# Performance work log

Hardware: AMD Instinct MI355X
Metric: run time of the kernel (lower is better)

Reference implementation:

```python
import jax, jax.numpy as jnp
import numpy as np

N_NODES = 20000   # graph nodes (rows of x)
N_EDGES = 40000
NUM_ENT = 300000  # node_count: embedding table rows
EMB_DIM = 64
D = 2 * EMB_DIM           # self.emb_dim = 128
SE = int(0.36 * D)        # s_emb_dim = 46
TE = D - SE               # t_emb_dim = 82
F = 256                   # raw feature cols of x
HID = 128                 # n_hidden
OUT = 2


def setup_inputs() -> dict:
    key = jax.random.key(0)
    ks = jax.random.split(key, 24)
    def nrm(k, shape, fan_in):
        return jax.random.normal(k, shape, jnp.float32) / np.sqrt(fan_in)
    inp = {
        'x': jax.random.normal(ks[0], (N_NODES, F), jnp.float32),
        'heads': jax.random.randint(ks[1], (N_EDGES,), 0, NUM_ENT),
        'rels': jax.random.randint(ks[2], (N_EDGES,), 0, 4),
        'tails': jax.random.randint(ks[3], (N_EDGES,), 0, NUM_ENT),
        'weeks': jax.random.uniform(ks[4], (N_EDGES,), jnp.float32),
        'edge_src': jnp.sort(jax.random.randint(ks[5], (N_EDGES,), 0, N_NODES)),
        'edge_dst': jax.random.randint(ks[6], (N_EDGES,), 0, N_NODES),
        'node_type': jax.random.randint(ks[7], (N_NODES,), 0, 5),
        'edge_type': jax.random.randint(ks[8], (N_EDGES,), 0, 4),
        'edge_index': jax.random.randint(ks[9], (2, N_EDGES), 0, N_NODES),
        # learned parameters
        'ent_embs': nrm(ks[10], (NUM_ENT, SE), SE),
        'rel_embs': nrm(ks[11], (4, D), D),
        'w_freq': nrm(ks[12], (NUM_ENT, TE), TE),
        'w_phi': nrm(ks[13], (NUM_ENT, TE), TE),
        'w_amp': nrm(ks[14], (NUM_ENT, TE), TE),
        'Wih': nrm(ks[15], (4 * D, D), D),
        'Whh': nrm(ks[16], (4 * D, D), D),
        'bih': jnp.zeros((4 * D,), jnp.float32),
        'bhh': jnp.zeros((4 * D,), jnp.float32),
        'fc1_w': nrm(ks[17], (HID, F + D), F + D),
        'fc1_b': jnp.zeros((HID,), jnp.float32),
        'ln_g': jnp.ones((HID,), jnp.float32),
        'ln_b': jnp.zeros((HID,), jnp.float32),
        'out_w': nrm(ks[18], (OUT, HID), HID),
        'out_b': jnp.zeros((OUT,), jnp.float32),
    }
    return inp


def _lstm_last_per_segment(pre, seg, Whh, bhh):
    """Run one LSTM over edges sorted by seg, resetting state at group
    boundaries; return per-step hidden states and the scatter index that
    selects the last step of each group (others map to dummy row N_NODES).
    pre: [E, 4D] precomputed x @ Wih^T + bih (sorted by seg)."""
    reset = jnp.concatenate([jnp.ones((1,), bool), seg[1:] != seg[:-1]])
    def step(carry, inp):
        h, c = carry
        p, r = inp
        h = jnp.where(r, 0.0, h)
        c = jnp.where(r, 0.0, c)
        gates = p + h @ Whh.T + bhh
        i, f, g, o = jnp.split(gates, 4, axis=-1)
        c = jax.nn.sigmoid(f) * c + jax.nn.sigmoid(i) * jnp.tanh(g)
        h = jax.nn.sigmoid(o) * jnp.tanh(c)
        return (h, c), h
    zero = jnp.zeros((D,), pre.dtype)
    _, hs = jax.lax.scan(step, (zero, zero), (pre, reset))
    is_last = jnp.concatenate([seg[1:] != seg[:-1], jnp.ones((1,), bool)])
    idx = jnp.where(is_last, seg, N_NODES)  # dummy row for non-last steps
    return hs, idx


def reference(x, heads, rels, tails, weeks, edge_src, edge_dst, node_type,
              edge_type, edge_index, ent_embs, rel_embs, w_freq, w_phi, w_amp,
              Wih, Whh, bih, bhh, fc1_w, fc1_b, ln_g, ln_b, out_w, out_b):
    week = weeks.reshape(-1, 1)  # [E,1]
    # getEmbeddings: static entity emb + diachronic (amp*sin(freq*t+phi)) part
    h_t = w_amp[heads] * jnp.sin(w_freq[heads] * week + w_phi[heads])
    t_t = w_amp[tails] * jnp.sin(w_freq[tails] * week + w_phi[tails])
    h = jnp.concatenate([ent_embs[heads], h_t], axis=1)  # [E, D]
    t = jnp.concatenate([ent_embs[tails], t_t], axis=1)  # [E, D]
    r = rel_embs[rels]                                    # [E, D]
    scores = h * r * t                                    # [E, D]

    # Ragged per-group LSTM (src groups, then dst groups overwrite), fused
    # as a single segment-reset scan per pass. Input projection hoisted.
    pre = scores @ Wih.T + bih  # [E, 4D]
    emb = jnp.zeros((N_NODES + 1, D), scores.dtype)
    perm_s = jnp.argsort(edge_src)  # stable
    hs, idx = _lstm_last_per_segment(pre[perm_s], edge_src[perm_s], Whh, bhh)
    emb = emb.at[idx].set(hs)
    perm_d = jnp.argsort(edge_dst)
    hs, idx = _lstm_last_per_segment(pre[perm_d], edge_dst[perm_d], Whh, bhh)
    emb = emb.at[idx].set(hs)
    emb = emb[:N_NODES]

    # (hgtconv2 omitted: GeneralConv source unavailable; treated as identity)
    xc = jnp.concatenate([x, emb], axis=1)  # mask = arange(N): all rows
    h1 = xc @ fc1_w.T + fc1_b
    mu = jnp.mean(h1, axis=-1, keepdims=True)
    var = jnp.mean((h1 - mu) ** 2, axis=-1, keepdims=True)
    h1 = (h1 - mu) / jnp.sqrt(var + 1e-5) * ln_g + ln_b
    h1 = jax.nn.relu(h1)  # dropout: eval mode, identity
    return h1 @ out_w.T + out_b
```

## Files before the change

kernel.cpp:

```cpp
#include <hip/hip_runtime.h>
#include <math.h>

#define N_NODES 20000
#define N_EDGES 40000
#define SE 46
#define TE 82
#define NBLK 79

typedef short  s16x8 __attribute__((ext_vector_type(8)));
typedef short  s16x4 __attribute__((ext_vector_type(4)));
typedef float  f32x4 __attribute__((ext_vector_type(4)));

__device__ __forceinline__ float sigf(float x){ return 1.0f/(1.0f+__expf(-x)); }
__device__ __forceinline__ float tanh_f(float x){ return 1.0f - 2.0f/(__expf(2.0f*x)+1.0f); }
__device__ __forceinline__ int perm_out(int i){ return (i&3)*128 + (i>>2); }
__device__ __forceinline__ unsigned short f2bf(float f){
  unsigned u = __builtin_bit_cast(unsigned, f);
  unsigned r = (u + 0x7fff + ((u>>16)&1)) >> 16;
  return (unsigned short)r;
}
__device__ __forceinline__ float bf2f(short s){
  unsigned u = ((unsigned)(unsigned short)s) << 16;
  return __builtin_bit_cast(float, u);
}

__global__ void k_prep(const float* __restrict__ Wih, const float* __restrict__ Whh,
                       const float* __restrict__ fc1w,
                       short* __restrict__ WihB, short* __restrict__ WhhB2,
                       short* __restrict__ fc1wbf){
  int idx = blockIdx.x*blockDim.x + threadIdx.x;
  if (idx < 65536){
    int i = idx >> 7, k = idx & 127;
    WihB[idx] = (short)f2bf(Wih[perm_out(i)*128 + k]);
  } else if (idx < 131072){
    int j = idx - 65536;
    WhhB2[j] = (short)f2bf(Whh[j]);
  } else if (idx < 180224){
    int j = idx - 131072;
    fc1wbf[j] = (short)f2bf(fc1w[j]);
  }
}

__global__ __launch_bounds__(256) void k_gather(
    const int* __restrict__ heads, const int* __restrict__ rels,
    const int* __restrict__ tails, const float* __restrict__ weeks,
    const float* __restrict__ ent, const float* __restrict__ rel_embs,
    const float* __restrict__ wfreq, const float* __restrict__ wphi,
    const float* __restrict__ wamp, short* __restrict__ scores){
  int c = blockIdx.x*256 + threadIdx.x;
  int e = c >> 4, d0 = (c & 15) << 3;
  int hd = heads[e], tl = tails[e], rl = rels[e];
  float wk = weeks[e];
  float hv[8], tv[8];
  if (d0 + 8 <= SE){
    const float* hp = ent + (size_t)hd*SE + d0;
    const float* tp = ent + (size_t)tl*SE + d0;
    #pragma unroll
    for (int j=0;j<4;j++){
      float2 a = *(const float2*)(hp + j*2); hv[2*j]=a.x; hv[2*j+1]=a.y;
      float2 b = *(const float2*)(tp + j*2); tv[2*j]=b.x; tv[2*j+1]=b.y;
    }
  } else if (d0 >= 48){
    int dt = d0 - SE;
    const float *hf = wfreq + (size_t)hd*TE + dt, *hp2 = wphi + (size_t)hd*TE + dt, *ha = wamp + (size_t)hd*TE + dt;
    const float *tf = wfreq + (size_t)tl*TE + dt, *tp2 = wphi + (size_t)tl*TE + dt, *ta = wamp + (size_t)tl*TE + dt;
    #pragma unroll
    for (int j=0;j<4;j++){
      float2 f_h = *(const float2*)(hf + j*2);
      float2 p_h = *(const float2*)(hp2 + j*2);
      float2 a_h = *(const float2*)(ha + j*2);
      float2 f_t = *(const float2*)(tf + j*2);
      float2 p_t = *(const float2*)(tp2 + j*2);
      float2 a_t = *(const float2*)(ta + j*2);
      hv[2*j]   = a_h.x*__sinf(f_h.x*wk + p_h.x);
      hv[2*j+1] = a_h.y*__sinf(f_h.y*wk + p_h.y);
      tv[2*j]   = a_t.x*__sinf(f_t.x*wk + p_t.x);
      tv[2*j+1] = a_t.y*__sinf(f_t.y*wk + p_t.y);
    }
  } else {
    #pragma unroll
    for (int j=0;j<8;j++){
      int d = 40 + j;
      if (d < SE){
        hv[j] = ent[(size_t)hd*SE + d];
        tv[j] = ent[(size_t)tl*SE + d];
      } else {
        int dt = d - SE;
        hv[j] = wamp[(size_t)hd*TE+dt]*__sinf(wfreq[(size_t)hd*TE+dt]*wk + wphi[(size_t)hd*TE+dt]);
        tv[j] = wamp[(size_t)tl*TE+dt]*__sinf(wfreq[(size_t)tl*TE+dt]*wk + wphi[(size_t)tl*TE+dt]);
      }
    }
  }
  const float* rp = rel_embs + rl*128 + d0;
  float4 r0 = *(const float4*)rp, r1 = *(const float4*)(rp+4);
  float rv[8] = {r0.x,r0.y,r0.z,r0.w, r1.x,r1.y,r1.z,r1.w};
  s16x8 o;
  #pragma unroll
  for (int j=0;j<8;j++) o[j] = (short)f2bf(hv[j]*rv[j]*tv[j]);
  *(s16x8*)(scores + (size_t)e*128 + d0) = o;
}

__global__ __launch_bounds__(256) void k_pregemm(
    const short* __restrict__ scores, const short* __restrict__ WihB,
    const float* __restrict__ bih, const float* __restrict__ bhh,
    short* __restrict__ pre2b){
  __shared__ char As[32*256];
  int e0 = blockIdx.x * 32;
  int tid = threadIdx.x;
  #pragma unroll
  for (int q=0;q<2;q++){
    int c = tid + 256*q;
    int el = c >> 4, k8 = c & 15;
    s16x8 v = *(const s16x8*)(scores + (size_t)(e0+el)*128 + k8*8);
    *(s16x8*)(As + ((el*256 + k8*16) ^ ((el&7)<<4))) = v;
  }
  __syncthreads();
  int lane = tid & 63, w = tid >> 6;
  int cl = lane & 15, kq = lane >> 4;
  s16x8 a[2][4];
  #pragma unroll
  for (int ks=0;ks<4;ks++){
    int kb = ks*64 + kq*16;
    a[0][ks] = *(const s16x8*)(As + (((cl   )*256 + kb) ^ ((cl&7)<<4)));
    a[1][ks] = *(const s16x8*)(As + (((cl+16)*256 + kb) ^ (((cl+16)&7)<<4)));
  }
  f32x4 D[2][8];
  #pragma unroll
  for (int m=0;m<2;m++)
    #pragma unroll
    for (int i=0;i<8;i++) D[m][i] = (f32x4){0.f,0.f,0.f,0.f};
  #pragma unroll
  for (int i=0;i<8;i++){
    int n = w*128 + i*16 + cl;
    const short* bp = WihB + (size_t)n*128 + kq*8;
    #pragma unroll
    for (int ks=0;ks<4;ks++){
      s16x8 b = *(const s16x8*)(bp + ks*32);
      D[0][i] = __builtin_amdgcn_mfma_f32_16x16x32_bf16(a[0][ks], b, D[0][i], 0, 0, 0);
      D[1][i] = __builtin_amdgcn_mfma_f32_16x16x32_bf16(a[1][ks], b, D[1][i], 0, 0, 0);
    }
  }
  #pragma unroll
  for (int i=0;i<8;i++){
    int n = w*128 + i*16 + cl;
    int pn = perm_out(n);
    float bb = bih[pn] + bhh[pn];
    #pragma unroll
    for (int m=0;m<2;m++){
      #pragma unroll
      for (int q2=0;q2<4;q2++){
        int row = m*16 + kq*4 + q2;
        pre2b[(size_t)(e0+row)*512 + n] = (short)f2bf(D[m][i][q2] + bb);
      }
    }
  }
}

__global__ void k_hist(const int* __restrict__ src, const int* __restrict__ dst,
                       int* __restrict__ scnt, int* __restrict__ dcnt){
  int e = blockIdx.x*blockDim.x + threadIdx.x;
  if (e < N_EDGES){ atomicAdd(&scnt[src[e]],1); atomicAdd(&dcnt[dst[e]],1); }
}

__global__ void k_scan(const int* __restrict__ scnt, const int* __restrict__ dcnt,
                       int* __restrict__ sstart, int* __restrict__ dstart){
  const int* cnt = blockIdx.x ? dcnt : scnt;
  int* start = blockIdx.x ? dstart : sstart;
  const int CH = 20;
  int tid = threadIdx.x;
  int base = tid*CH;
  int v[CH]; int tsum = 0;
  #pragma unroll
  for (int j=0;j<CH;j++){ int i = base+j; v[j] = (i<N_NODES)? cnt[i] : 0; tsum += v[j]; }
  int lane = tid & 63, wv = tid >> 6;
  int incl = tsum;
  #pragma unroll
  for (int m=1;m<64;m<<=1){ int u = __shfl_up(incl, m); if (lane >= m) incl += u; }
  __shared__ int wsum[16], woff[16];
  if (lane==63) wsum[wv] = incl;
  __syncthreads();
  if (tid < 16){ int s=0; for (int k=0;k<tid;k++) s += wsum[k]; woff[tid]=s; }
  __syncthreads();
  int run = woff[wv] + incl - tsum;
  #pragma unroll
  for (int j=0;j<CH;j++){ int i = base+j; if (i<N_NODES) start[i] = run; run += v[j]; }
  if (tid == 1023) start[N_NODES] = run;
}

__global__ void k_scatter(const int* __restrict__ src, const int* __restrict__ dst,
                          const int* __restrict__ sstart, const int* __restrict__ dstart,
                          int* __restrict__ sc2, int* __restrict__ dc2,
                          int* __restrict__ slist, int* __restrict__ dlist){
  int e = blockIdx.x*blockDim.x + threadIdx.x;
  if (e < N_EDGES){
    int s = src[e]; int p  = sstart[s] + atomicAdd(&sc2[s],1); slist[p]=e;
    int d = dst[e]; int p2 = dstart[d] + atomicAdd(&dc2[d],1); dlist[p2]=e;
  }
}

__global__ void k_sortlists(const int* __restrict__ sstart, const int* __restrict__ dstart,
                            int* __restrict__ slist, int* __restrict__ dlist){
  int n = blockIdx.x*blockDim.x + threadIdx.x;
  if (n < N_NODES){
    #pragma unroll
    for (int pass=0; pass<2; pass++){
      const int* st = pass ? dstart : sstart;
      int* ls = pass ? dlist : slist;
      int a = st[n], b = st[n+1];
      for (int i=a+1;i<b;i++){
        int v = ls[i]; int j=i-1;
        while (j>=a && ls[j]>v){ ls[j+1]=ls[j]; j--; }
        ls[j+1]=v;
      }
    }
  }
}

__global__ void k_cbin1(const int* __restrict__ sstart, const int* __restrict__ dstart,
                        int* __restrict__ bhist){
  __shared__ int h[128];
  int tid = threadIdx.x, blk = blockIdx.x;
  if (tid < 128) h[tid] = 0;
  __syncthreads();
  int n = blk*256 + tid;
  if (n < N_NODES){
    int c  = sstart[n+1]-sstart[n];
    int c2 = dstart[n+1]-dstart[n];
    if (c>0 && c2==0) atomicAdd(&h[min(c,63)], 1);
    if (c2>0) atomicAdd(&h[64+min(c2,63)], 1);
  }
  __syncthreads();
  if (tid < 128) bhist[tid*NBLK + blk] = h[tid];
}

__global__ void k_cbin2(const int* __restrict__ bhist, int* __restrict__ boff,
                        int* __restrict__ nchains){
  const int S = 2*63*NBLK;
  const int CH = 10;
  int tid = threadIdx.x;
  int v[CH]; int tsum = 0;
  int binidx[CH];
  #pragma unroll
  for (int j=0;j<CH;j++){
    int s = tid*CH + j;
    int val = 0, bi = -1;
    if (s < S){
      int p = s / (63*NBLK);
      int r = s - p*63*NBLK;
      int li = r / NBLK;
      int b  = r - li*NBLK;
      int l  = 63 - li;
      bi = (p*64 + l)*NBLK + b;
      val = bhist[bi];
    }
    binidx[j] = bi; v[j] = val; tsum += val;
  }
  int lane = tid & 63, wv = tid >> 6;
  int incl = tsum;
  #pragma unroll
  for (int m=1;m<64;m<<=1){ int u = __shfl_up(incl, m); if (lane >= m) incl += u; }
  __shared__ int wsum[16], woff[16];
  __shared__ int pend[2];
  if (lane==63) wsum[wv] = incl;
  __syncthreads();
  if (tid < 16){ int s=0; for (int k=0;k<tid;k++) s += wsum[k]; woff[tid]=s; }
  __syncthreads();
  int run = woff[wv] + incl - tsum;
  #pragma unroll
  for (int j=0;j<CH;j++){
    int s = tid*CH + j;
    if (s < S){
      boff[binidx[j]] = run;
      run += v[j];
      if (s == 63*NBLK - 1) pend[0] = run;
      if (s == S - 1)       pend[1] = run;
    }
  }
  __syncthreads();
  if (tid == 0){
    nchains[0] = pend[0];
    nchains[1] = pend[1] - pend[0];
  }
}

__global__ void k_cbin3(const int* __restrict__ sstart, const int* __restrict__ dstart,
                        const int* __restrict__ boff, const int* __restrict__ nchains,
                        int* __restrict__ cnode, int* __restrict__ cstart,
                        int* __restrict__ clen){
  __shared__ int h[128];
  int tid = threadIdx.x, blk = blockIdx.x;
  if (tid < 128) h[tid] = 0;
  __syncthreads();
  int n = blk*256 + tid;
  int bin0=-1, bin1=-1, r0=0, r1=0, a0=0, c0=0, a1=0, c1=0;
  if (n < N_NODES){
    a0 = sstart[n]; c0 = sstart[n+1]-a0;
    a1 = dstart[n]; c1 = dstart[n+1]-a1;
    if (c0>0 && c1==0){ bin0 = min(c0,63);    r0 = atomicAdd(&h[bin0], 1); }
    if (c1>0)         { bin1 = 64+min(c1,63); r1 = atomicAdd(&h[bin1], 1); }
  }
  __syncthreads();
  int nch0 = nchains[0];
  if (bin0 >= 0){
    int pos = boff[bin0*NBLK + blk] + r0;
    cnode[pos] = n; cstart[pos] = a0; clen[pos] = c0;
  }
  if (bin1 >= 0){
    int pos = boff[bin1*NBLK + blk] + r1 - nch0;
    cnode[N_NODES+pos] = n; cstart[N_NODES+pos] = a1; clen[N_NODES+pos] = c1;
  }
}

__global__ __launch_bounds__(512, 1) void k_lstm6(
    const short* __restrict__ pre2b, const short* __restrict__ WhhB2,
    const int* __restrict__ cnode, const int* __restrict__ cstart,
    const int* __restrict__ clen, const int* __restrict__ nchains,
    const int* __restrict__ slist, const int* __restrict__ dlist,
    int* __restrict__ ctr, float* __restrict__ emb){
  __shared__ char Hb[2][8192];
  __shared__ int M[161];
  int tid = threadIdx.x;
  int lane = tid & 63, wv = tid >> 6;
  int cl = lane & 15, kq = lane >> 4;
  int d_own = wv*16 + cl;
  s16x8 wf[4][4];
  #pragma unroll
  for (int i=0;i<4;i++)
    #pragma unroll
    for (int ks=0;ks<4;ks++)
      wf[i][ks] = *(const s16x8*)(WhhB2 + (size_t)(i*128 + d_own)*128 + ks*32 + kq*8);
  int nch0 = nchains[0], nch1 = nchains[1];
  int B0 = (nch0+31)>>5, B1 = (nch1+31)>>5;
  while (true){
    if (tid==0) M[160] = atomicAdd(ctr, 1);
    __syncthreads();
    int nb = M[160];
    if (nb >= B0 + B1) break;
    int pass = (nb >= B0) ? 1 : 0;
    int batch = pass ? nb - B0 : nb;
    int b0 = batch << 5;
    int nch = pass ? nch1 : nch0;
    const int* list = pass ? dlist : slist;
    if (tid < 32){
      int j = b0 + tid;
      int valid = (j < nch);
      int ci = pass*N_NODES + j;
      int st = valid ? cstart[ci] : 0;
      int ln = valid ? clen[ci] : 0;
      M[tid] = ln; M[32+tid] = st; M[128+tid] = valid ? cnode[ci] : -1;
      M[64+tid] = (ln > 0) ? list[st]   : 0;
      M[96+tid] = (ln > 1) ? list[st+1] : 0;
    }
    *(unsigned long long*)(&Hb[0][tid*16])   = 0ull;
    *(unsigned long long*)(&Hb[0][tid*16+8]) = 0ull;
    float cst[8]  = {0.f,0.f,0.f,0.f,0.f,0.f,0.f,0.f};
    float hreg[8] = {0.f,0.f,0.f,0.f,0.f,0.f,0.f,0.f};
    __syncthreads();
    int mylen[8];
    #pragma unroll
    for (int m=0;m<2;m++)
      #pragma unroll
      for (int q=0;q<4;q++) mylen[m*4+q] = M[m*16 + kq*4 + q];
    int ml = 0;
    #pragma unroll 1
    for (int j=0;j<32;j++) ml = max(ml, M[j]);
    s16x4 pvc[8];
    #pragma unroll
    for (int m=0;m<2;m++)
      #pragma unroll
      for (int q=0;q<4;q++){
        int r = m*16 + kq*4 + q;
        pvc[m*4+q] = *(const s16x4*)(pre2b + (size_t)M[64+r]*512 + d_own*4);
      }
    int cur = 0;
    for (int t=0; t<ml; t++){
      s16x4 pvn[8];
      const int* eidN = M + 64 + (((t+1)&1)<<5);
      #pragma unroll
      for (int m=0;m<2;m++)
        #pragma unroll
        for (int q=0;q<4;q++){
          int r = m*16 + kq*4 + q;
          pvn[m*4+q] = *(const s16x4*)(pre2b + (size_t)eidN[r]*512 + d_own*4);
        }
      f32x4 D[2][4];
      #pragma unroll
      for (int m=0;m<2;m++)
        #pragma unroll
        for (int i=0;i<4;i++) D[m][i] = (f32x4){0.f,0.f,0.f,0.f};
      char* Hc = Hb[cur];
      #pragma unroll
      for (int ks=0; ks<4; ks++){
        int kb = ks*64 + kq*16;
        s16x8 a0 = *(const s16x8*)(Hc + (((cl   )*256 + kb) ^ ((cl&7)<<4)));
        s16x8 a1 = *(const s16x8*)(Hc + (((cl+16)*256 + kb) ^ (((cl+16)&7)<<4)));
        #pragma unroll
        for (int i=0;i<4;i++){
          D[0][i] = __builtin_amdgcn_mfma_f32_16x16x32_bf16(a0, wf[i][ks], D[0][i], 0, 0, 0);
          D[1][i] = __builtin_amdgcn_mfma_f32_16x16x32_bf16(a1, wf[i][ks], D[1][i], 0, 0, 0);
        }
      }
      char* Hn = Hb[cur^1];
      #pragma unroll
      for (int m=0;m<2;m++)
        #pragma unroll
        for (int q=0;q<4;q++){
          int r = m*16 + kq*4 + q;
          if (t < mylen[m*4+q]){
            s16x4 p = pvc[m*4+q];
            float gi = D[m][0][q] + bf2f(p[0]);
            float gf = D[m][1][q] + bf2f(p[1]);
            float gg = D[m][2][q] + bf2f(p[2]);
            float go = D[m][3][q] + bf2f(p[3]);
            int idx = m*4+q;
            cst[idx] = sigf(gf)*cst[idx] + sigf(gi)*tanh_f(gg);
            float h = sigf(go)*tanh_f(cst[idx]);
            hreg[idx] = h;
            *(short*)(Hn + ((r*256 + d_own*2) ^ ((r&7)<<4))) = (short)f2bf(h);
          }
        }
      if (tid < 32){
        int ln = M[tid];
        M[64 + ((t&1)<<5) + tid] = (t+2 < ln) ? list[M[32+tid] + t+2] : 0;
      }
      __syncthreads();
      #pragma unroll
      for (int i=0;i<8;i++) pvc[i] = pvn[i];
      cur ^= 1;
    }
    #pragma unroll
    for (int m=0;m<2;m++)
      #pragma unroll
      for (int q=0;q<4;q++){
        int r = m*16 + kq*4 + q;
        int n = M[128+r];
        if (mylen[m*4+q] > 0 && n >= 0){
          emb[(size_t)n*128 + d_own] = hreg[m*4+q];
        }
      }
    __syncthreads();
  }
}

__global__ __launch_bounds__(512) void k_mlp2(
    const float* __restrict__ x, const float* __restrict__ emb,
    const short* __restrict__ fc1wbf, const float* __restrict__ fc1b,
    const float* __restrict__ lng, const float* __restrict__ lnb,
    const float* __restrict__ outw, const float* __restrict__ outb,
    float* __restrict__ out){
  __shared__ char As[32*768];
  __shared__ float hbuf[32][132];
  int tid = threadIdx.x;
  int lane = tid & 63, w = tid >> 6;
  int base = blockIdx.x * 32;
  #pragma unroll
  for (int q=0;q<3;q++){
    int i = tid + 512*q;
    int r = i / 48, c = i - r*48;
    const float* src = (c < 32) ? (x + (size_t)(base+r)*256 + c*8)
                                : (emb + (size_t)(base+r)*128 + (c-32)*8);
    float4 v0 = *(const float4*)src;
    float4 v1 = *(const float4*)(src+4);
    s16x8 v8;
    v8[0]=(short)f2bf(v0.x); v8[1]=(short)f2bf(v0.y); v8[2]=(short)f2bf(v0.z); v8[3]=(short)f2bf(v0.w);
    v8[4]=(short)f2bf(v1.x); v8[5]=(short)f2bf(v1.y); v8[6]=(short)f2bf(v1.z); v8[7]=(short)f2bf(v1.w);
    *(s16x8*)(As + ((r*768 + c*16) ^ ((r&7)<<4))) = v8;
  }
  __syncthreads();
  int cl = lane & 15, kq = lane >> 4;
  f32x4 D0 = {0.f,0.f,0.f,0.f}, D1 = {0.f,0.f,0.f,0.f};
  const short* bp = fc1wbf + (size_t)(w*16 + cl)*384 + kq*8;
  #pragma unroll
  for (int ks=0; ks<12; ks++){
    s16x8 b = *(const s16x8*)(bp + ks*32);
    int kb = ks*64 + kq*16;
    s16x8 a0 = *(const s16x8*)(As + (((cl   )*768 + kb) ^ ((cl&7)<<4)));
    s16x8 a1 = *(const s16x8*)(As + (((cl+16)*768 + kb) ^ (((cl+16)&7)<<4)));
    D0 = __builtin_amdgcn_mfma_f32_16x16x32_bf16(a0, b, D0, 0, 0, 0);
    D1 = __builtin_amdgcn_mfma_f32_16x16x32_bf16(a1, b, D1, 0, 0, 0);
  }
  int col = w*16 + cl;
  float bb = fc1b[col];
  #pragma unroll
  for (int q=0;q<4;q++){
    hbuf[kq*4+q][col]    = D0[q] + bb;
    hbuf[16+kq*4+q][col] = D1[q] + bb;
  }
  __syncthreads();
  int sub = lane >> 4, l16 = lane & 15;
  int nd = w*4 + sub;
  float v[8];
  float s = 0.f;
  #pragma unroll
  for (int j=0;j<8;j++){ v[j] = hbuf[nd][l16*8+j]; s += v[j]; }
  #pragma unroll
  for (int m=1;m<16;m<<=1) s += __shfl_xor(s, m);
  float mu = s * (1.f/128.f);
  float va = 0.f;
  #pragma unroll
  for (int j=0;j<8;j++){ float dm = v[j]-mu; va += dm*dm; }
  #pragma unroll
  for (int m=1;m<16;m<<=1) va += __shfl_xor(va, m);
  float rstd = rsqrtf(va*(1.f/128.f) + 1e-5f);
  float o0=0.f, o1=0.f;
  #pragma unroll
  for (int j=0;j<8;j++){
    int c = l16*8+j;
    float h1 = (v[j]-mu)*rstd*lng[c] + lnb[c];
    h1 = fmaxf(h1, 0.f);
    o0 += h1*outw[c]; o1 += h1*outw[128+c];
  }
  #pragma unroll
  for (int m=1;m<16;m<<=1){ o0 += __shfl_xor(o0,m); o1 += __shfl_xor(o1,m); }
  if (l16==0){
    out[(size_t)(base+nd)*2]   = o0 + outb[0];
    out[(size_t)(base+nd)*2+1] = o1 + outb[1];
  }
}

extern "C" void kernel_launch(void* const* d_in, const int* in_sizes, int n_in,
                              void* d_out, int out_size, void* d_ws, size_t ws_size,
                              hipStream_t stream){
  const float* x      = (const float*)d_in[0];
  const int*   heads  = (const int*)d_in[1];
  const int*   rels   = (const int*)d_in[2];
  const int*   tails  = (const int*)d_in[3];
  const float* weeks  = (const float*)d_in[4];
  const int*   esrc   = (const int*)d_in[5];
  const int*   edst   = (const int*)d_in[6];
  const float* ent    = (const float*)d_in[10];
  const float* rel_e  = (const float*)d_in[11];
  const float* wfreq  = (const float*)d_in[12];
  const float* wphi   = (const float*)d_in[13];
  const float* wamp   = (const float*)d_in[14];
  const float* Wih    = (const float*)d_in[15];
  const float* Whh    = (const float*)d_in[16];
  const float* bih    = (const float*)d_in[17];
  const float* bhh    = (const float*)d_in[18];
  const float* fc1w   = (const float*)d_in[19];
  const float* fc1b   = (const float*)d_in[20];
  const float* lng    = (const float*)d_in[21];
  const float* lnb    = (const float*)d_in[22];
  const float* outw   = (const float*)d_in[23];
  const float* outb   = (const float*)d_in[24];
  float* out = (float*)d_out;

  char* ws = (char*)d_ws;
  size_t off = 0;
  auto alloc = [&](size_t bytes){ void* p = ws + off; off += (bytes + 255) & ~(size_t)255; return p; };
  short* pre2b  = (short*)alloc((size_t)N_EDGES*512*2);
  short* scores = (short*)alloc((size_t)N_EDGES*128*2);
  short* WihB   = (short*)alloc(512*128*2);
  short* WhhB2  = (short*)alloc(512*128*2);
  short* fc1wbf = (short*)alloc(128*384*2);
  float* emb    = (float*)alloc((size_t)N_NODES*128*4);
  int* sstart   = (int*)alloc((N_NODES+1)*4);
  int* dstart   = (int*)alloc((N_NODES+1)*4);
  int* zreg     = (int*)alloc((size_t)(4*N_NODES + 3)*4);
  int* scnt = zreg, *dcnt = zreg+N_NODES, *sc2 = zreg+2*N_NODES, *dc2 = zreg+3*N_NODES;
  int* nchains  = zreg + 4*N_NODES;
  int* ctr      = nchains + 2;
  int* bhist    = (int*)alloc((size_t)128*NBLK*4);
  int* boff     = (int*)alloc((size_t)128*NBLK*4);
  int* slist    = (int*)alloc(N_EDGES*4);
  int* dlist    = (int*)alloc(N_EDGES*4);
  int* cnode    = (int*)alloc((size_t)2*N_NODES*4);
  int* cstart   = (int*)alloc((size_t)2*N_NODES*4);
  int* clen     = (int*)alloc((size_t)2*N_NODES*4);

  hipMemsetAsync(zreg, 0, (size_t)(4*N_NODES + 3)*4, stream);
  hipMemsetAsync(emb, 0, (size_t)N_NODES*128*4, stream);

  k_prep<<<(180224+255)/256, 256, 0, stream>>>(Wih, Whh, fc1w, WihB, WhhB2, fc1wbf);

  k_gather<<<N_EDGES*16/256, 256, 0, stream>>>(heads, rels, tails, weeks, ent, rel_e,
                                               wfreq, wphi, wamp, scores);
  k_pregemm<<<N_EDGES/32, 256, 0, stream>>>(scores, WihB, bih, bhh, pre2b);
  k_hist<<<(N_EDGES+255)/256, 256, 0, stream>>>(esrc, edst, scnt, dcnt);
  k_scan<<<2, 1024, 0, stream>>>(scnt, dcnt, sstart, dstart);
  k_scatter<<<(N_EDGES+255)/256, 256, 0, stream>>>(esrc, edst, sstart, dstart, sc2, dc2, slist, dlist);
  k_sortlists<<<(N_NODES+255)/256, 256, 0, stream>>>(sstart, dstart, slist, dlist);
  k_cbin1<<<NBLK, 256, 0, stream>>>(sstart, dstart, bhist);
  k_cbin2<<<1, 1024, 0, stream>>>(bhist, boff, nchains);
  k_cbin3<<<NBLK, 256, 0, stream>>>(sstart, dstart, boff, nchains, cnode, cstart, clen);
  k_lstm6<<<256, 512, 0, stream>>>(pre2b, WhhB2, cnode, cstart, clen, nchains,
                                   slist, dlist, ctr, emb);
  k_mlp2<<<N_NODES/32, 512, 0, stream>>>(x, emb, fc1wbf, fc1b, lng, lnb, outw, outb, out);
}
```

Measured before the change: 181.1 us.

## Merge front-end kernels, drop src list build and emb memset

Gather, weight conversion and histogram now run as one launch, and the scatter, sort and chain-binning steps are merged into fewer launches. Because edge_src is already sorted, the src edge list is no longer built and its position is used as the edge id directly. The emb memset is replaced by a per-node degree flag that k_mlp2 checks before reading emb, and the next-edge prefetch in the LSTM loop moves earlier. This cuts launch count and memory traffic, but relies on edge_src being sorted in the input and adds an extra barrier inside the LSTM setup.

```diff
diff --git a/kernel.cpp b/kernel.cpp
--- a/kernel.cpp
+++ b/kernel.cpp
@@ -24,80 +24,91 @@
   return __builtin_bit_cast(float, u);
 }
 
-__global__ void k_prep(const float* __restrict__ Wih, const float* __restrict__ Whh,
-                       const float* __restrict__ fc1w,
-                       short* __restrict__ WihB, short* __restrict__ WhhB2,
-                       short* __restrict__ fc1wbf){
-  int idx = blockIdx.x*blockDim.x + threadIdx.x;
-  if (idx < 65536){
-    int i = idx >> 7, k = idx & 127;
-    WihB[idx] = (short)f2bf(Wih[perm_out(i)*128 + k]);
-  } else if (idx < 131072){
-    int j = idx - 65536;
-    WhhB2[j] = (short)f2bf(Whh[j]);
-  } else if (idx < 180224){
-    int j = idx - 131072;
-    fc1wbf[j] = (short)f2bf(fc1w[j]);
-  }
-}
-
-__global__ __launch_bounds__(256) void k_gather(
+#define GATHER_BLKS 2500
+#define PREP_BLKS   704
+#define HIST_BLKS   157
+#define FRONT_BLKS  (GATHER_BLKS + PREP_BLKS + HIST_BLKS)
+
+__global__ __launch_bounds__(256) void k_front(
     const int* __restrict__ heads, const int* __restrict__ rels,
     const int* __restrict__ tails, const float* __restrict__ weeks,
     const float* __restrict__ ent, const float* __restrict__ rel_embs,
     const float* __restrict__ wfreq, const float* __restrict__ wphi,
-    const float* __restrict__ wamp, short* __restrict__ scores){
-  int c = blockIdx.x*256 + threadIdx.x;
-  int e = c >> 4, d0 = (c & 15) << 3;
-  int hd = heads[e], tl = tails[e], rl = rels[e];
-  float wk = weeks[e];
-  float hv[8], tv[8];
-  if (d0 + 8 <= SE){
-    const float* hp = ent + (size_t)hd*SE + d0;
-    const float* tp = ent + (size_t)tl*SE + d0;
-    #pragma unroll
-    for (int j=0;j<4;j++){
-      float2 a = *(const float2*)(hp + j*2); hv[2*j]=a.x; hv[2*j+1]=a.y;
-      float2 b = *(const float2*)(tp + j*2); tv[2*j]=b.x; tv[2*j+1]=b.y;
-    }
-  } else if (d0 >= 48){
-    int dt = d0 - SE;
-    const float *hf = wfreq + (size_t)hd*TE + dt, *hp2 = wphi + (size_t)hd*TE + dt, *ha = wamp + (size_t)hd*TE + dt;
-    const float *tf = wfreq + (size_t)tl*TE + dt, *tp2 = wphi + (size_t)tl*TE + dt, *ta = wamp + (size_t)tl*TE + dt;
-    #pragma unroll
-    for (int j=0;j<4;j++){
-      float2 f_h = *(const float2*)(hf + j*2);
-      float2 p_h = *(const float2*)(hp2 + j*2);
-      float2 a_h = *(const float2*)(ha + j*2);
-      float2 f_t = *(const float2*)(tf + j*2);
-      float2 p_t = *(const float2*)(tp2 + j*2);
-      float2 a_t = *(const float2*)(ta + j*2);
-      hv[2*j]   = a_h.x*__sinf(f_h.x*wk + p_h.x);
-      hv[2*j+1] = a_h.y*__sinf(f_h.y*wk + p_h.y);
-      tv[2*j]   = a_t.x*__sinf(f_t.x*wk + p_t.x);
-      tv[2*j+1] = a_t.y*__sinf(f_t.y*wk + p_t.y);
+    const float* __restrict__ wamp, short* __restrict__ scores,
+    const float* __restrict__ Wih, const float* __restrict__ Whh,
+    const float* __restrict__ fc1w,
+    short* __restrict__ WihB, short* __restrict__ WhhB2, short* __restrict__ fc1wbf,
+    const int* __restrict__ esrc, const int* __restrict__ edst,
+    int* __restrict__ scnt, int* __restrict__ dcnt){
+  int blk = blockIdx.x, tid = threadIdx.x;
+  if (blk < GATHER_BLKS){
+    int c = blk*256 + tid;
+    int e = c >> 4, d0 = (c & 15) << 3;
+    int hd = heads[e], tl = tails[e], rl = rels[e];
+    float wk = weeks[e];
+    float hv[8], tv[8];
+    if (d0 + 8 <= SE){
+      const float* hp = ent + (size_t)hd*SE + d0;
+      const float* tp = ent + (size_t)tl*SE + d0;
+      #pragma unroll
+      for (int j=0;j<4;j++){
+        float2 a = *(const float2*)(hp + j*2); hv[2*j]=a.x; hv[2*j+1]=a.y;
+        float2 b = *(const float2*)(tp + j*2); tv[2*j]=b.x; tv[2*j+1]=b.y;
+      }
+    } else if (d0 >= 48){
+      int dt = d0 - SE;
+      const float *hf = wfreq + (size_t)hd*TE + dt, *hp2 = wphi + (size_t)hd*TE + dt, *ha = wamp + (size_t)hd*TE + dt;
+      const float *tf = wfreq + (size_t)tl*TE + dt, *tp2 = wphi + (size_t)tl*TE + dt, *ta = wamp + (size_t)tl*TE + dt;
+      #pragma unroll
+      for (int j=0;j<4;j++){
+        float2 f_h = *(const float2*)(hf + j*2);
+        float2 p_h = *(const float2*)(hp2 + j*2);
+        float2 a_h = *(const float2*)(ha + j*2);
+        float2 f_t = *(const float2*)(tf + j*2);
+        float2 p_t = *(const float2*)(tp2 + j*2);
+        float2 a_t = *(const float2*)(ta + j*2);
+        hv[2*j]   = a_h.x*__sinf(f_h.x*wk + p_h.x);
+        hv[2*j+1] = a_h.y*__sinf(f_h.y*wk + p_h.y);
+        tv[2*j]   = a_t.x*__sinf(f_t.x*wk + p_t.x);
+        tv[2*j+1] = a_t.y*__sinf(f_t.y*wk + p_t.y);
+      }
+    } else {
+      #pragma unroll
+      for (int j=0;j<8;j++){
+        int d = 40 + j;
+        if (d < SE){
+          hv[j] = ent[(size_t)hd*SE + d];
+          tv[j] = ent[(size_t)tl*SE + d];
+        } else {
+          int dt = d - SE;
+          hv[j] = wamp[(size_t)hd*TE+dt]*__sinf(wfreq[(size_t)hd*TE+dt]*wk + wphi[(size_t)hd*TE+dt]);
+          tv[j] = wamp[(size_t)tl*TE+dt]*__sinf(wfreq[(size_t)tl*TE+dt]*wk + wphi[(size_t)tl*TE+dt]);
+        }
+      }
+    }
+    const float* rp = rel_embs + rl*128 + d0;
+    float4 r0 = *(const float4*)rp, r1 = *(const float4*)(rp+4);
+    float rv[8] = {r0.x,r0.y,r0.z,r0.w, r1.x,r1.y,r1.z,r1.w};
+    s16x8 o;
+    #pragma unroll
+    for (int j=0;j<8;j++) o[j] = (short)f2bf(hv[j]*rv[j]*tv[j]);
+    *(s16x8*)(scores + (size_t)e*128 + d0) = o;
+  } else if (blk < GATHER_BLKS + PREP_BLKS){
+    int idx = (blk - GATHER_BLKS)*256 + tid;
+    if (idx < 65536){
+      int i = idx >> 7, k = idx & 127;
+      WihB[idx] = (short)f2bf(Wih[perm_out(i)*128 + k]);
+    } else if (idx < 131072){
+      int j = idx - 65536;
+      WhhB2[j] = (short)f2bf(Whh[j]);
+    } else if (idx < 180224){
+      int j = idx - 131072;
+      fc1wbf[j] = (short)f2bf(fc1w[j]);
     }
   } else {
-    #pragma unroll
-    for (int j=0;j<8;j++){
-      int d = 40 + j;
-      if (d < SE){
-        hv[j] = ent[(size_t)hd*SE + d];
-        tv[j] = ent[(size_t)tl*SE + d];
-      } else {
-        int dt = d - SE;
-        hv[j] = wamp[(size_t)hd*TE+dt]*__sinf(wfreq[(size_t)hd*TE+dt]*wk + wphi[(size_t)hd*TE+dt]);
-        tv[j] = wamp[(size_t)tl*TE+dt]*__sinf(wfreq[(size_t)tl*TE+dt]*wk + wphi[(size_t)tl*TE+dt]);
-      }
-    }
-  }
-  const float* rp = rel_embs + rl*128 + d0;
-  float4 r0 = *(const float4*)rp, r1 = *(const float4*)(rp+4);
-  float rv[8] = {r0.x,r0.y,r0.z,r0.w, r1.x,r1.y,r1.z,r1.w};
-  s16x8 o;
-  #pragma unroll
-  for (int j=0;j<8;j++) o[j] = (short)f2bf(hv[j]*rv[j]*tv[j]);
-  *(s16x8*)(scores + (size_t)e*128 + d0) = o;
+    int e = (blk - GATHER_BLKS - PREP_BLKS)*256 + tid;
+    if (e < N_EDGES){ atomicAdd(&scnt[esrc[e]],1); atomicAdd(&dcnt[edst[e]],1); }
+  }
 }
 
 __global__ __launch_bounds__(256) void k_pregemm(
@@ -154,12 +165,6 @@
       }
     }
   }
-}
-
-__global__ void k_hist(const int* __restrict__ src, const int* __restrict__ dst,
-                       int* __restrict__ scnt, int* __restrict__ dcnt){
-  int e = blockIdx.x*blockDim.x + threadIdx.x;
-  if (e < N_EDGES){ atomicAdd(&scnt[src[e]],1); atomicAdd(&dcnt[dst[e]],1); }
 }
 
 __global__ void k_scan(const int* __restrict__ scnt, const int* __restrict__ dcnt,
@@ -187,106 +192,99 @@
   if (tid == 1023) start[N_NODES] = run;
 }
 
-__global__ void k_scatter(const int* __restrict__ src, const int* __restrict__ dst,
-                          const int* __restrict__ sstart, const int* __restrict__ dstart,
-                          int* __restrict__ sc2, int* __restrict__ dc2,
-                          int* __restrict__ slist, int* __restrict__ dlist){
-  int e = blockIdx.x*blockDim.x + threadIdx.x;
-  if (e < N_EDGES){
-    int s = src[e]; int p  = sstart[s] + atomicAdd(&sc2[s],1); slist[p]=e;
-    int d = dst[e]; int p2 = dstart[d] + atomicAdd(&dc2[d],1); dlist[p2]=e;
-  }
-}
-
-__global__ void k_sortlists(const int* __restrict__ sstart, const int* __restrict__ dstart,
-                            int* __restrict__ slist, int* __restrict__ dlist){
-  int n = blockIdx.x*blockDim.x + threadIdx.x;
-  if (n < N_NODES){
-    #pragma unroll
-    for (int pass=0; pass<2; pass++){
-      const int* st = pass ? dstart : sstart;
-      int* ls = pass ? dlist : slist;
-      int a = st[n], b = st[n+1];
+__global__ __launch_bounds__(256) void k_scatcb1(
+    const int* __restrict__ edst, const int* __restrict__ dstart,
+    int* __restrict__ dc2, int* __restrict__ dlist,
+    const int* __restrict__ sstart, int* __restrict__ bhist){
+  int blk = blockIdx.x, tid = threadIdx.x;
+  if (blk < HIST_BLKS){
+    int e = blk*256 + tid;
+    if (e < N_EDGES){
+      int d = edst[e]; int p2 = dstart[d] + atomicAdd(&dc2[d],1); dlist[p2]=e;
+    }
+  } else {
+    __shared__ int h[128];
+    int b2 = blk - HIST_BLKS;
+    if (tid < 128) h[tid] = 0;
+    __syncthreads();
+    int n = b2*256 + tid;
+    if (n < N_NODES){
+      int c  = sstart[n+1]-sstart[n];
+      int c2 = dstart[n+1]-dstart[n];
+      if (c>0 && c2==0) atomicAdd(&h[min(c,63)], 1);
+      if (c2>0) atomicAdd(&h[64+min(c2,63)], 1);
+    }
+    __syncthreads();
+    if (tid < 128) bhist[tid*NBLK + b2] = h[tid];
+  }
+}
+
+__device__ __forceinline__ int mapbin(int s){
+  int p = s / (63*NBLK);
+  int r = s - p*63*NBLK;
+  int li = r / NBLK;
+  int b  = r - li*NBLK;
+  int l  = 63 - li;
+  return (p*64 + l)*NBLK + b;
+}
+
+__global__ __launch_bounds__(256) void k_sortcb2(
+    const int* __restrict__ dstart, int* __restrict__ dlist,
+    const int* __restrict__ bhist, int* __restrict__ boff,
+    int* __restrict__ nchains){
+  int blk = blockIdx.x, tid = threadIdx.x;
+  __shared__ int wsum[4];
+  __shared__ int pend[2];
+  if (blk < NBLK){
+    int n = blk*256 + tid;
+    if (n < N_NODES){
+      int a = dstart[n], b = dstart[n+1];
       for (int i=a+1;i<b;i++){
-        int v = ls[i]; int j=i-1;
-        while (j>=a && ls[j]>v){ ls[j+1]=ls[j]; j--; }
-        ls[j+1]=v;
-      }
-    }
-  }
-}
-
-__global__ void k_cbin1(const int* __restrict__ sstart, const int* __restrict__ dstart,
-                        int* __restrict__ bhist){
-  __shared__ int h[128];
-  int tid = threadIdx.x, blk = blockIdx.x;
-  if (tid < 128) h[tid] = 0;
-  __syncthreads();
-  int n = blk*256 + tid;
-  if (n < N_NODES){
-    int c  = sstart[n+1]-sstart[n];
-    int c2 = dstart[n+1]-dstart[n];
-    if (c>0 && c2==0) atomicAdd(&h[min(c,63)], 1);
-    if (c2>0) atomicAdd(&h[64+min(c2,63)], 1);
-  }
-  __syncthreads();
-  if (tid < 128) bhist[tid*NBLK + blk] = h[tid];
-}
-
-__global__ void k_cbin2(const int* __restrict__ bhist, int* __restrict__ boff,
-                        int* __restrict__ nchains){
-  const int S = 2*63*NBLK;
-  const int CH = 10;
-  int tid = threadIdx.x;
-  int v[CH]; int tsum = 0;
-  int binidx[CH];
-  #pragma unroll
-  for (int j=0;j<CH;j++){
-    int s = tid*CH + j;
-    int val = 0, bi = -1;
-    if (s < S){
-      int p = s / (63*NBLK);
-      int r = s - p*63*NBLK;
-      int li = r / NBLK;
-      int b  = r - li*NBLK;
-      int l  = 63 - li;
-      bi = (p*64 + l)*NBLK + b;
-      val = bhist[bi];
-    }
-    binidx[j] = bi; v[j] = val; tsum += val;
-  }
-  int lane = tid & 63, wv = tid >> 6;
-  int incl = tsum;
-  #pragma unroll
-  for (int m=1;m<64;m<<=1){ int u = __shfl_up(incl, m); if (lane >= m) incl += u; }
-  __shared__ int wsum[16], woff[16];
-  __shared__ int pend[2];
-  if (lane==63) wsum[wv] = incl;
-  __syncthreads();
-  if (tid < 16){ int s=0; for (int k=0;k<tid;k++) s += wsum[k]; woff[tid]=s; }
-  __syncthreads();
-  int run = woff[wv] + incl - tsum;
-  #pragma unroll
-  for (int j=0;j<CH;j++){
-    int s = tid*CH + j;
-    if (s < S){
-      boff[binidx[j]] = run;
-      run += v[j];
-      if (s == 63*NBLK - 1) pend[0] = run;
-      if (s == S - 1)       pend[1] = run;
-    }
-  }
-  __syncthreads();
-  if (tid == 0){
-    nchains[0] = pend[0];
-    nchains[1] = pend[1] - pend[0];
+        int v = dlist[i]; int j=i-1;
+        while (j>=a && dlist[j]>v){ dlist[j+1]=dlist[j]; j--; }
+        dlist[j+1]=v;
+      }
+    }
+  } else {
+    const int S = 2*63*NBLK;
+    const int CH2 = 39;
+    int tsum = 0;
+    for (int j=0;j<CH2;j++){
+      int s = tid*CH2 + j;
+      if (s < S) tsum += bhist[mapbin(s)];
+    }
+    int lane = tid & 63, wv = tid >> 6;
+    int incl = tsum;
+    #pragma unroll
+    for (int m=1;m<64;m<<=1){ int u = __shfl_up(incl, m); if (lane >= m) incl += u; }
+    if (lane==63) wsum[wv] = incl;
+    __syncthreads();
+    int woff = 0;
+    for (int k=0;k<wv;k++) woff += wsum[k];
+    int run = woff + incl - tsum;
+    for (int j=0;j<CH2;j++){
+      int s = tid*CH2 + j;
+      if (s < S){
+        int bi = mapbin(s);
+        int val = bhist[bi];
+        boff[bi] = run;
+        run += val;
+        if (s == 63*NBLK - 1) pend[0] = run;
+        if (s == S - 1)       pend[1] = run;
+      }
+    }
+    __syncthreads();
+    if (tid == 0){
+      nchains[0] = pend[0];
+      nchains[1] = pend[1] - pend[0];
+    }
   }
 }
 
 __global__ void k_cbin3(const int* __restrict__ sstart, const int* __restrict__ dstart,
                         const int* __restrict__ boff, const int* __restrict__ nchains,
                         int* __restrict__ cnode, int* __restrict__ cstart,
-                        int* __restrict__ clen){
+                        int* __restrict__ clen, int* __restrict__ degf){
   __shared__ int h[128];
   int tid = threadIdx.x, blk = blockIdx.x;
   if (tid < 128) h[tid] = 0;
@@ -296,6 +294,7 @@
   if (n < N_NODES){
     a0 = sstart[n]; c0 = sstart[n+1]-a0;
     a1 = dstart[n]; c1 = dstart[n+1]-a1;
+    degf[n] = (c0+c1 > 0) ? 1 : 0;
     if (c0>0 && c1==0){ bin0 = min(c0,63);    r0 = atomicAdd(&h[bin0], 1); }
     if (c1>0)         { bin1 = 64+min(c1,63); r1 = atomicAdd(&h[bin1], 1); }
   }
@@ -311,12 +310,12 @@
   }
 }
 
-__global__ __launch_bounds__(512, 1) void k_lstm6(
+__global__ __launch_bounds__(512, 1) void k_lstm7(
     const short* __restrict__ pre2b, const short* __restrict__ WhhB2,
     const int* __restrict__ cnode, const int* __restrict__ cstart,
     const int* __restrict__ clen, const int* __restrict__ nchains,
-    const int* __restrict__ slist, const int* __restrict__ dlist,
-    int* __restrict__ ctr, float* __restrict__ emb){
+    const int* __restrict__ dlist, int* __restrict__ ctr,
+    float* __restrict__ emb){
   __shared__ char Hb[2][8192];
   __shared__ int M[161];
   int tid = threadIdx.x;
@@ -340,7 +339,6 @@
     int batch = pass ? nb - B0 : nb;
     int b0 = batch << 5;
     int nch = pass ? nch1 : nch0;
-    const int* list = pass ? dlist : slist;
     if (tid < 32){
       int j = b0 + tid;
       int valid = (j < nch);
@@ -348,8 +346,8 @@
       int st = valid ? cstart[ci] : 0;
       int ln = valid ? clen[ci] : 0;
       M[tid] = ln; M[32+tid] = st; M[128+tid] = valid ? cnode[ci] : -1;
-      M[64+tid] = (ln > 0) ? list[st]   : 0;
-      M[96+tid] = (ln > 1) ? list[st+1] : 0;
+      M[64+tid] = (ln > 0) ? (pass ? dlist[st]   : st  ) : 0;
+      M[96+tid] = (ln > 1) ? (pass ? dlist[st+1] : st+1) : 0;
     }
     *(unsigned long long*)(&Hb[0][tid*16])   = 0ull;
     *(unsigned long long*)(&Hb[0][tid*16+8]) = 0ull;
@@ -372,8 +370,14 @@
         int r = m*16 + kq*4 + q;
         pvc[m*4+q] = *(const s16x4*)(pre2b + (size_t)M[64+r]*512 + d_own*4);
       }
+    __syncthreads();
     int cur = 0;
     for (int t=0; t<ml; t++){
+      if (tid < 32){
+        int ln = M[tid];
+        int nxt = M[32+tid] + t + 2;
+        M[64 + ((t&1)<<5) + tid] = (t+2 < ln) ? (pass ? dlist[nxt] : nxt) : 0;
+      }
       s16x4 pvn[8];
       const int* eidN = M + 64 + (((t+1)&1)<<5);
       #pragma unroll
@@ -419,10 +423,6 @@
             *(short*)(Hn + ((r*256 + d_own*2) ^ ((r&7)<<4))) = (short)f2bf(h);
           }
         }
-      if (tid < 32){
-        int ln = M[tid];
-        M[64 + ((t&1)<<5) + tid] = (t+2 < ln) ? list[M[32+tid] + t+2] : 0;
-      }
       __syncthreads();
       #pragma unroll
       for (int i=0;i<8;i++) pvc[i] = pvn[i];
@@ -444,6 +444,7 @@
 
 __global__ __launch_bounds__(512) void k_mlp2(
     const float* __restrict__ x, const float* __restrict__ emb,
+    const int* __restrict__ degf,
     const short* __restrict__ fc1wbf, const float* __restrict__ fc1b,
     const float* __restrict__ lng, const float* __restrict__ lnb,
     const float* __restrict__ outw, const float* __restrict__ outb,
@@ -457,13 +458,20 @@
   for (int q=0;q<3;q++){
     int i = tid + 512*q;
     int r = i / 48, c = i - r*48;
-    const float* src = (c < 32) ? (x + (size_t)(base+r)*256 + c*8)
-                                : (emb + (size_t)(base+r)*128 + (c-32)*8);
-    float4 v0 = *(const float4*)src;
-    float4 v1 = *(const float4*)(src+4);
-    s16x8 v8;
-    v8[0]=(short)f2bf(v0.x); v8[1]=(short)f2bf(v0.y); v8[2]=(short)f2bf(v0.z); v8[3]=(short)f2bf(v0.w);
-    v8[4]=(short)f2bf(v1.x); v8[5]=(short)f2bf(v1.y); v8[6]=(short)f2bf(v1.z); v8[7]=(short)f2bf(v1.w);
+    s16x8 v8 = {0,0,0,0,0,0,0,0};
+    if (c < 32){
+      const float* src = x + (size_t)(base+r)*256 + c*8;
+      float4 v0 = *(const float4*)src;
+      float4 v1 = *(const float4*)(src+4);
+      v8[0]=(short)f2bf(v0.x); v8[1]=(short)f2bf(v0.y); v8[2]=(short)f2bf(v0.z); v8[3]=(short)f2bf(v0.w);
+      v8[4]=(short)f2bf(v1.x); v8[5]=(short)f2bf(v1.y); v8[6]=(short)f2bf(v1.z); v8[7]=(short)f2bf(v1.w);
+    } else if (degf[base+r]){
+      const float* src = emb + (size_t)(base+r)*128 + (c-32)*8;
+      float4 v0 = *(const float4*)src;
+      float4 v1 = *(const float4*)(src+4);
+      v8[0]=(short)f2bf(v0.x); v8[1]=(short)f2bf(v0.y); v8[2]=(short)f2bf(v0.z); v8[3]=(short)f2bf(v0.w);
+      v8[4]=(short)f2bf(v1.x); v8[5]=(short)f2bf(v1.y); v8[6]=(short)f2bf(v1.z); v8[7]=(short)f2bf(v1.w);
+    }
     *(s16x8*)(As + ((r*768 + c*16) ^ ((r&7)<<4))) = v8;
   }
   __syncthreads();
@@ -556,34 +564,30 @@
   float* emb    = (float*)alloc((size_t)N_NODES*128*4);
   int* sstart   = (int*)alloc((N_NODES+1)*4);
   int* dstart   = (int*)alloc((N_NODES+1)*4);
-  int* zreg     = (int*)alloc((size_t)(4*N_NODES + 3)*4);
-  int* scnt = zreg, *dcnt = zreg+N_NODES, *sc2 = zreg+2*N_NODES, *dc2 = zreg+3*N_NODES;
-  int* nchains  = zreg + 4*N_NODES;
+  int* zreg     = (int*)alloc((size_t)(3*N_NODES + 3)*4);
+  int* scnt = zreg, *dcnt = zreg+N_NODES, *dc2 = zreg+2*N_NODES;
+  int* nchains  = zreg + 3*N_NODES;
   int* ctr      = nchains + 2;
   int* bhist    = (int*)alloc((size_t)128*NBLK*4);
   int* boff     = (int*)alloc((size_t)128*NBLK*4);
-  int* slist    = (int*)alloc(N_EDGES*4);
   int* dlist    = (int*)alloc(N_EDGES*4);
   int* cnode    = (int*)alloc((size_t)2*N_NODES*4);
   int* cstart   = (int*)alloc((size_t)2*N_NODES*4);
   int* clen     = (int*)alloc((size_t)2*N_NODES*4);
-
-  hipMemsetAsync(zreg, 0, (size_t)(4*N_NODES + 3)*4, stream);
-  hipMemsetAsync(emb, 0, (size_t)N_NODES*128*4, stream);
-
-  k_prep<<<(180224+255)/256, 256, 0, stream>>>(Wih, Whh, fc1w, WihB, WhhB2, fc1wbf);
-
-  k_gather<<<N_EDGES*16/256, 256, 0, stream>>>(heads, rels, tails, weeks, ent, rel_e,
-                                               wfreq, wphi, wamp, scores);
+  int* degf     = (int*)alloc((size_t)N_NODES*4);
+
+  hipMemsetAsync(zreg, 0, (size_t)(3*N_NODES + 3)*4, stream);
+
+  k_front<<<FRONT_BLKS, 256, 0, stream>>>(heads, rels, tails, weeks, ent, rel_e,
+                                          wfreq, wphi, wamp, scores,
+                                          Wih, Whh, fc1w, WihB, WhhB2, fc1wbf,
+                                          esrc, edst, scnt, dcnt);
   k_pregemm<<<N_EDGES/32, 256, 0, stream>>>(scores, WihB, bih, bhh, pre2b);
-  k_hist<<<(N_EDGES+255)/256, 256, 0, stream>>>(esrc, edst, scnt, dcnt);
   k_scan<<<2, 1024, 0, stream>>>(scnt, dcnt, sstart, dstart);
-  k_scatter<<<(N_EDGES+255)/256, 256, 0, stream>>>(esrc, edst, sstart, dstart, sc2, dc2, slist, dlist);
-  k_sortlists<<<(N_NODES+255)/256, 256, 0, stream>>>(sstart, dstart, slist, dlist);
-  k_cbin1<<<NBLK, 256, 0, stream>>>(sstart, dstart, bhist);
-  k_cbin2<<<1, 1024, 0, stream>>>(bhist, boff, nchains);
-  k_cbin3<<<NBLK, 256, 0, stream>>>(sstart, dstart, boff, nchains, cnode, cstart, clen);
-  k_lstm6<<<256, 512, 0, stream>>>(pre2b, WhhB2, cnode, cstart, clen, nchains,
-                                   slist, dlist, ctr, emb);
-  k_mlp2<<<N_NODES/32, 512, 0, stream>>>(x, emb, fc1wbf, fc1b, lng, lnb, outw, outb, out);
-}
+  k_scatcb1<<<HIST_BLKS + NBLK, 256, 0, stream>>>(edst, dstart, dc2, dlist, sstart, bhist);
+  k_sortcb2<<<NBLK + 1, 256, 0, stream>>>(dstart, dlist, bhist, boff, nchains);
+  k_cbin3<<<NBLK, 256, 0, stream>>>(sstart, dstart, boff, nchains, cnode, cstart, clen, degf);
+  k_lstm7<<<256, 512, 0, stream>>>(pre2b, WhhB2, cnode, cstart, clen, nchains,
+                                   dlist, ctr, emb);
+  k_mlp2<<<N_NODES/32, 512, 0, stream>>>(x, emb, degf, fc1wbf, fc1b, lng, lnb, outw, outb, out);
+}
```

New measurement: 170.4 us. -5.9%, faster.
